# Kernel optimization log

Measured on AMD Instinct MI355X. Metric: run time of the kernel, lower is better.

The kernel has to match this reference:

```python
import jax, jax.numpy as jnp
import numpy as np

B, N, IN, H = 8, 2048, 256, 128
ALPHA = 0.2  # leaky relu slope


def setup_inputs() -> dict:
    key = jax.random.key(0)
    k1, k2, k3, k4 = jax.random.split(key, 4)
    x = jax.random.normal(k1, (B, N, IN), dtype=jnp.float32)
    # adj_identity: batched identity matrix (masks self-attention, then re-adds weight-1 self loop)
    adj_identity = jnp.broadcast_to(jnp.eye(N, dtype=jnp.float32), (B, N, N))
    W = jax.random.normal(k2, (H, IN), dtype=jnp.float32) * (1.0 / np.sqrt(IN))
    b = jnp.zeros((H,), dtype=jnp.float32)
    # atten_fact: [2H, 1], xavier_normal with gain=1.414
    std = 1.414 * np.sqrt(2.0 / (2 * H + 1))
    a = jax.random.normal(k3, (2 * H, 1), dtype=jnp.float32) * std
    return {"input": x, "adj_identity": adj_identity, "W": W, "b": b, "a": a}


def reference(input, adj_identity, W, b, a):
    # input projection: [B,N,H]
    h = jnp.einsum("bni,hi->bnh", input, W) + b
    # decomposition of cat([h_i, h_j]) @ a == h_i@a1 + h_j@a2 (exact same math,
    # avoids materializing the [B, N*N, 2H] tensor)
    a1 = a[:H, 0]  # [H]
    a2 = a[H:, 0]  # [H]
    si = h @ a1  # [B,N]
    sj = h @ a2  # [B,N]
    scores = jax.nn.leaky_relu(si[:, :, None] + sj[:, None, :], negative_slope=ALPHA)  # [B,N,N]
    scores = jnp.where(adj_identity != 0, -jnp.inf, scores)
    attn = jax.nn.softmax(scores, axis=-1) + adj_identity  # [B,N,N]
    # dropout p=0.0 -> identity
    out = jax.nn.elu(jnp.einsum("bnm,bmh->bnh", attn, h))
    return out
```

## Files before the change

### kernel.cpp

```cpp
#include <hip/hip_runtime.h>
#include <hip/hip_bf16.h>
#include <cmath>


#define ALPHA 0.2f
#define NN 2048
#define NIN 256
#define NH 128

typedef __attribute__((ext_vector_type(8))) short short8;
typedef __attribute__((ext_vector_type(4))) float f32x4;

__device__ __forceinline__ unsigned int pk2(float a, float b) {
    unsigned int r;
    asm("v_cvt_pk_bf16_f32 %0, %1, %2" : "=v"(r) : "v"(a), "v"(b));
    return r;
}

__global__ __launch_bounds__(256) void k1_h(
    const float* __restrict__ x, const float* __restrict__ Wm,
    const float* __restrict__ bias, const float* __restrict__ av,
    float* __restrict__ si, float* __restrict__ sj,
    unsigned short* __restrict__ hTt)
{
    __shared__ __align__(16) unsigned short xls[64 * 264];
    __shared__ __align__(16) unsigned short Wls[128 * 264];
    __shared__ float a1l[128], a2l[128], bl[128];

    const int t = threadIdx.x;
    const int r0 = blockIdx.x * 64;

    for (int p = 0; p < 16; ++p) {
        int idx = p * 256 + t;
        int row = idx >> 6, kq = idx & 63;
        f32x4 v = *(const f32x4*)(x + (size_t)(r0 + row) * NIN + kq * 4);
        *(uint2*)(&xls[row * 264 + kq * 4]) = make_uint2(pk2(v[0], v[1]), pk2(v[2], v[3]));
    }
    for (int p = 0; p < 32; ++p) {
        int idx = p * 256 + t;
        int row = idx >> 6, kq = idx & 63;
        f32x4 v = *(const f32x4*)(Wm + (size_t)row * NIN + kq * 4);
        *(uint2*)(&Wls[row * 264 + kq * 4]) = make_uint2(pk2(v[0], v[1]), pk2(v[2], v[3]));
    }
    if (t < 128) { a1l[t] = av[t]; a2l[t] = av[128 + t]; bl[t] = bias[t]; }
    __syncthreads();

    const int w = t >> 6, l = t & 63, la = l & 15, g = l >> 4;

    f32x4 acc[8];
#pragma unroll
    for (int n = 0; n < 8; ++n) acc[n] = (f32x4){0.f, 0.f, 0.f, 0.f};

#pragma unroll
    for (int ks = 0; ks < 8; ++ks) {
        short8 af = *(const short8*)(&xls[(w * 16 + la) * 264 + ks * 32 + g * 8]);
#pragma unroll
        for (int n = 0; n < 8; ++n) {
            short8 bfr = *(const short8*)(&Wls[(n * 16 + la) * 264 + ks * 32 + g * 8]);
            acc[n] = __builtin_amdgcn_mfma_f32_16x16x32_bf16(af, bfr, acc[n], 0, 0, 0);
        }
    }

    float s1[4] = {0.f, 0.f, 0.f, 0.f}, s2[4] = {0.f, 0.f, 0.f, 0.f};
#pragma unroll
    for (int n = 0; n < 8; ++n) {
        int col = n * 16 + la;
#pragma unroll
        for (int r = 0; r < 4; ++r) {
            float v = acc[n][r] + bl[col];
            acc[n][r] = v;
            s1[r] += v * a1l[col];
            s2[r] += v * a2l[col];
        }
    }
#pragma unroll
    for (int r = 0; r < 4; ++r) {
#pragma unroll
        for (int m = 1; m < 16; m <<= 1) {
            s1[r] += __shfl_xor(s1[r], m, 64);
            s2[r] += __shfl_xor(s2[r], m, 64);
        }
    }
    if (la == 0) {
#pragma unroll
        for (int r = 0; r < 4; ++r) {
            int row = w * 16 + g * 4 + r;
            si[r0 + row] = s1[r];
            sj[r0 + row] = s2[r];
        }
    }

    __syncthreads();
    unsigned short* oT = xls;
#pragma unroll
    for (int n = 0; n < 8; ++n) {
        int col = n * 16 + la;
        int row0 = w * 16 + g * 4;
        *(uint2*)(&oT[col * 72 + row0]) =
            make_uint2(pk2(acc[n][0], acc[n][1]), pk2(acc[n][2], acc[n][3]));
    }
    __syncthreads();
    const int b = r0 >> 11, jt = (r0 & (NN - 1)) >> 6;
    unsigned short* dst = hTt + ((size_t)(b * 32 + jt)) * 8192;
    for (int p = 0; p < 4; ++p) {
        int idx = p * 256 + t;
        int col = idx >> 3, seg = idx & 7;
        uint4 v = *(const uint4*)(&oT[col * 72 + seg * 8]);
        *(uint4*)(dst + col * 64 + seg * 8) = v;
    }
}

__global__ __launch_bounds__(512) void k3_attn(
    const unsigned short* __restrict__ hTt,
    const float* __restrict__ si, const float* __restrict__ sj,
    float* __restrict__ out)
{
    __shared__ __align__(16) float f1l[NN];
    __shared__ __align__(16) float f2l[NN];
    __shared__ __align__(16) unsigned short hl[2][128 * 72];
    __shared__ float Zl[2][32];
    __shared__ float mr1[8], mr2[8];

    const int t = threadIdx.x;
    const int bb = blockIdx.x & 7;
    const int grp = blockIdx.x >> 3;
    const int i0 = grp * 32;
    const int w = t >> 6, l = t & 63;
    const int wr = (w >> 2) & 1;
    const int wcg = (w >> 1) & 1;
    const int wk = w & 1;
    const int la = l & 15, g = l >> 4;

    const unsigned short* tb = hTt + (size_t)bb * (32 * 8192);

    uint4 c0 = ((const uint4*)tb)[t];
    uint4 c1 = ((const uint4*)tb)[t + 512];

    ((f32x4*)f1l)[t] = ((const f32x4*)(sj + bb * NN))[t];
    __syncthreads();
    f32x4 vv = ((const f32x4*)f1l)[t];
    float m1, m2;
    {
        float hi0 = fmaxf(vv[0], vv[1]), lo0 = fminf(vv[0], vv[1]);
        float hi1 = fmaxf(vv[2], vv[3]), lo1 = fminf(vv[2], vv[3]);
        m1 = fmaxf(hi0, hi1);
        m2 = fmaxf(fminf(hi0, hi1), fmaxf(lo0, lo1));
    }
#pragma unroll
    for (int m = 1; m < 64; m <<= 1) {
        float o1 = __shfl_xor(m1, m, 64), o2 = __shfl_xor(m2, m, 64);
        float n1 = fmaxf(m1, o1);
        float n2 = fmaxf(fminf(m1, o1), fmaxf(m2, o2));
        m1 = n1; m2 = n2;
    }
    if (l == 0) { mr1[w] = m1; mr2[w] = m2; }
    __syncthreads();
    {
        float a1 = mr1[0], a2 = mr2[0];
#pragma unroll
        for (int wv2 = 1; wv2 < 8; ++wv2) {
            float b1 = mr1[wv2], b2 = mr2[wv2];
            float n1 = fmaxf(a1, b1), n2 = fmaxf(fminf(a1, b1), fmaxf(a2, b2));
            a1 = n1; a2 = n2;
        }
        m1 = a1; m2 = a2;
    }
    {
        f32x4 e1t, e2t;
#pragma unroll
        for (int u = 0; u < 4; ++u) { e1t[u] = expf(vv[u]); e2t[u] = expf(ALPHA * vv[u]); }
        ((f32x4*)f1l)[t] = e1t;
        ((f32x4*)f2l)[t] = e2t;
    }

    float e1v, e2v, owv;
    {
        int gi = bb * NN + i0 + wr * 16 + la;
        float svi = si[gi], svj = sj[gi];
        float M = (svj == m1) ? m2 : m1;
        float sm = svi + M;
        float mm = sm > 0.f ? sm : ALPHA * sm;
        float a = expf(svi - mm), b2 = expf(ALPHA * svi - mm);
        e1v = a; e2v = b2;
        float owr = fmaxf(a * expf(svj), b2 * expf(ALPHA * svj));
        owv = __uint_as_float(pk2(owr, owr) << 16);
    }

    f32x4 acc[4], zac;
    zac = (f32x4){0.f, 0.f, 0.f, 0.f};
#pragma unroll
    for (int n = 0; n < 4; ++n) acc[n] = (f32x4){0.f, 0.f, 0.f, 0.f};
    short8 ones;
#pragma unroll
    for (int u = 0; u < 8; ++u) ones[u] = (short)0x3F80;

    const int sidx0 = (t >> 3) * 72 + (t & 7) * 8;
    const int sidx1 = ((t + 512) >> 3) * 72 + (t & 7) * 8;

    for (int jt = 0; jt < 32; ++jt) {
        unsigned short* buf = hl[jt & 1];
        *(uint4*)(&buf[sidx0]) = c0;
        *(uint4*)(&buf[sidx1]) = c1;
        if (jt < 31) {
            const uint4* nt = (const uint4*)(tb + (size_t)(jt + 1) * 8192);
            c0 = nt[t];
            c1 = nt[t + 512];
        }
        __syncthreads();

        const int jb = jt * 64 + wk * 32 + g * 8;
        f32x4 F1a = *(const f32x4*)(f1l + jb);
        f32x4 F1b = *(const f32x4*)(f1l + jb + 4);
        f32x4 F2a = *(const f32x4*)(f2l + jb);
        f32x4 F2b = *(const f32x4*)(f2l + jb + 4);

        short8 af;
        {
            float w0 = fmaxf(e1v * F1a[0], e2v * F2a[0]);
            float w1 = fmaxf(e1v * F1a[1], e2v * F2a[1]);
            float w2 = fmaxf(e1v * F1a[2], e2v * F2a[2]);
            float w3 = fmaxf(e1v * F1a[3], e2v * F2a[3]);
            float w4 = fmaxf(e1v * F1b[0], e2v * F2b[0]);
            float w5 = fmaxf(e1v * F1b[1], e2v * F2b[1]);
            float w6 = fmaxf(e1v * F1b[2], e2v * F2b[2]);
            float w7 = fmaxf(e1v * F1b[3], e2v * F2b[3]);
            union { unsigned int u[4]; short8 s; } cv;
            cv.u[0] = pk2(w0, w1);
            cv.u[1] = pk2(w2, w3);
            cv.u[2] = pk2(w4, w5);
            cv.u[3] = pk2(w6, w7);
            af = cv.s;
        }
#pragma unroll
        for (int n = 0; n < 4; ++n) {
            const int col = wcg * 64 + n * 16 + la;
            short8 bfr = *(const short8*)(&buf[col * 72 + wk * 32 + g * 8]);
            acc[n] = __builtin_amdgcn_mfma_f32_16x16x32_bf16(af, bfr, acc[n], 0, 0, 0);
        }
        zac = __builtin_amdgcn_mfma_f32_16x16x32_bf16(af, ones, zac, 0, 0, 0);
    }

    __syncthreads();
    float* xch = (float*)hl;
    const int pair = wr * 2 + wcg;
    if (wk == 1) {
#pragma unroll
        for (int n = 0; n < 4; ++n)
#pragma unroll
            for (int r = 0; r < 4; ++r)
                xch[(n * 4 + r) * 256 + pair * 64 + l] = acc[n][r];
    }
    if (wcg == 0 && la == 0) {
#pragma unroll
        for (int r = 0; r < 4; ++r)
            Zl[wk][wr * 16 + g * 4 + r] = zac[r];
    }
    __syncthreads();

    if (wk == 0) {
#pragma unroll
        for (int n = 0; n < 4; ++n)
#pragma unroll
            for (int r = 0; r < 4; ++r)
                acc[n][r] += xch[(n * 4 + r) * 256 + pair * 64 + l];

        const int jt_res = grp >> 1;
        const int joff = (grp & 1) * 32;
#pragma unroll
        for (int n = 0; n < 4; ++n) {
            const int col = wcg * 64 + n * 16 + la;
#pragma unroll
            for (int r = 0; r < 4; ++r) {
                const int row = wr * 16 + g * 4 + r;
                const float Z = Zl[0][row] + Zl[1][row];
                const int srcl = (g * 4 + r) | (l & 48);
                const float owq = __shfl(owv, srcl, 64);
                const float hv = __uint_as_float(
                    (unsigned int)tb[jt_res * 8192 + col * 64 + joff + row] << 16);
                const float num = acc[n][r] - owq * hv;
                const float den = Z - owq;
                float o = num / den + hv;
                out[(size_t)(bb * NN + i0 + row) * NH + col] = o > 0.f ? o : expm1f(o);
            }
        }
    }
}

extern "C" void kernel_launch(void* const* d_in, const int* in_sizes, int n_in,
                              void* d_out, int out_size, void* d_ws, size_t ws_size,
                              hipStream_t stream)
{
    const float* x    = (const float*)d_in[0];
    const float* Wm   = (const float*)d_in[2];
    const float* bias = (const float*)d_in[3];
    const float* av   = (const float*)d_in[4];
    float* out = (float*)d_out;

    float* wsf = (float*)d_ws;
    unsigned short* hTt = (unsigned short*)wsf;
    float* si = wsf + 1048576;
    float* sj = wsf + 1064960;

    hipLaunchKernelGGL(k1_h,    dim3(256), dim3(256), 0, stream, x, Wm, bias, av, si, sj, hTt);
    hipLaunchKernelGGL(k3_attn, dim3(512), dim3(512), 0, stream, hTt, si, sj, out);
}
```

Measured before the change: 40.60 us.

## Split projection kernel across 8 waves by output column and stage W in halves

The projection kernel now runs 512 threads per block, with each wave owning 16 output columns across all 64 rows instead of 16 rows across all columns. W is converted and staged into shared memory in two K-halves to cut LDS footprint. The si/sj dot products are reduced across waves through a new shared buffer. This adds parallelism and lowers LDS use in the small first kernel, at the cost of an extra barrier and a cross-wave reduction.

```diff
diff --git a/kernel.cpp b/kernel.cpp
--- a/kernel.cpp
+++ b/kernel.cpp
@@ -17,96 +17,108 @@
     return r;
 }
 
-__global__ __launch_bounds__(256) void k1_h(
+__global__ __launch_bounds__(512) void k1_h(
     const float* __restrict__ x, const float* __restrict__ Wm,
     const float* __restrict__ bias, const float* __restrict__ av,
     float* __restrict__ si, float* __restrict__ sj,
     unsigned short* __restrict__ hTt)
 {
     __shared__ __align__(16) unsigned short xls[64 * 264];
-    __shared__ __align__(16) unsigned short Wls[128 * 264];
+    __shared__ __align__(16) unsigned short Wh[128 * 136];
     __shared__ float a1l[128], a2l[128], bl[128];
+    __shared__ float red1[8][64], red2[8][64];
 
     const int t = threadIdx.x;
     const int r0 = blockIdx.x * 64;
-
-    for (int p = 0; p < 16; ++p) {
-        int idx = p * 256 + t;
+    const int w = t >> 6, l = t & 63, la = l & 15, g = l >> 4;
+
+    for (int i = 0; i < 8; ++i) {
+        int idx = i * 512 + t;
         int row = idx >> 6, kq = idx & 63;
         f32x4 v = *(const f32x4*)(x + (size_t)(r0 + row) * NIN + kq * 4);
         *(uint2*)(&xls[row * 264 + kq * 4]) = make_uint2(pk2(v[0], v[1]), pk2(v[2], v[3]));
     }
-    for (int p = 0; p < 32; ++p) {
-        int idx = p * 256 + t;
-        int row = idx >> 6, kq = idx & 63;
-        f32x4 v = *(const f32x4*)(Wm + (size_t)row * NIN + kq * 4);
-        *(uint2*)(&Wls[row * 264 + kq * 4]) = make_uint2(pk2(v[0], v[1]), pk2(v[2], v[3]));
-    }
     if (t < 128) { a1l[t] = av[t]; a2l[t] = av[128 + t]; bl[t] = bias[t]; }
-    __syncthreads();
-
-    const int w = t >> 6, l = t & 63, la = l & 15, g = l >> 4;
-
-    f32x4 acc[8];
-#pragma unroll
-    for (int n = 0; n < 8; ++n) acc[n] = (f32x4){0.f, 0.f, 0.f, 0.f};
-
-#pragma unroll
-    for (int ks = 0; ks < 8; ++ks) {
-        short8 af = *(const short8*)(&xls[(w * 16 + la) * 264 + ks * 32 + g * 8]);
-#pragma unroll
-        for (int n = 0; n < 8; ++n) {
-            short8 bfr = *(const short8*)(&Wls[(n * 16 + la) * 264 + ks * 32 + g * 8]);
-            acc[n] = __builtin_amdgcn_mfma_f32_16x16x32_bf16(af, bfr, acc[n], 0, 0, 0);
-        }
-    }
-
-    float s1[4] = {0.f, 0.f, 0.f, 0.f}, s2[4] = {0.f, 0.f, 0.f, 0.f};
-#pragma unroll
-    for (int n = 0; n < 8; ++n) {
-        int col = n * 16 + la;
+
+    f32x4 acc[4];
+#pragma unroll
+    for (int fr = 0; fr < 4; ++fr) acc[fr] = (f32x4){0.f, 0.f, 0.f, 0.f};
+
+#pragma unroll
+    for (int kh = 0; kh < 2; ++kh) {
+        if (kh) __syncthreads();
+        for (int i = 0; i < 8; ++i) {
+            int idx = i * 512 + t;
+            int row = idx >> 5, kq = idx & 31;
+            f32x4 v = *(const f32x4*)(Wm + (size_t)row * NIN + kh * 128 + kq * 4);
+            *(uint2*)(&Wh[row * 136 + kq * 4]) = make_uint2(pk2(v[0], v[1]), pk2(v[2], v[3]));
+        }
+        __syncthreads();
+#pragma unroll
+        for (int ksl = 0; ksl < 4; ++ksl) {
+            short8 bfr = *(const short8*)(&Wh[(w * 16 + la) * 136 + ksl * 32 + g * 8]);
+#pragma unroll
+            for (int fr = 0; fr < 4; ++fr) {
+                short8 af = *(const short8*)(
+                    &xls[(fr * 16 + la) * 264 + kh * 128 + ksl * 32 + g * 8]);
+                acc[fr] = __builtin_amdgcn_mfma_f32_16x16x32_bf16(af, bfr, acc[fr], 0, 0, 0);
+            }
+        }
+    }
+
+    const int col = w * 16 + la;
+    float s1[4][4], s2[4][4];
+#pragma unroll
+    for (int fr = 0; fr < 4; ++fr)
 #pragma unroll
         for (int r = 0; r < 4; ++r) {
-            float v = acc[n][r] + bl[col];
-            acc[n][r] = v;
-            s1[r] += v * a1l[col];
-            s2[r] += v * a2l[col];
-        }
-    }
-#pragma unroll
-    for (int r = 0; r < 4; ++r) {
-#pragma unroll
-        for (int m = 1; m < 16; m <<= 1) {
-            s1[r] += __shfl_xor(s1[r], m, 64);
-            s2[r] += __shfl_xor(s2[r], m, 64);
-        }
-    }
+            float v = acc[fr][r] + bl[col];
+            acc[fr][r] = v;
+            s1[fr][r] = v * a1l[col];
+            s2[fr][r] = v * a2l[col];
+        }
+#pragma unroll
+    for (int m = 1; m < 16; m <<= 1)
+#pragma unroll
+        for (int fr = 0; fr < 4; ++fr)
+#pragma unroll
+            for (int r = 0; r < 4; ++r) {
+                s1[fr][r] += __shfl_xor(s1[fr][r], m, 64);
+                s2[fr][r] += __shfl_xor(s2[fr][r], m, 64);
+            }
     if (la == 0) {
 #pragma unroll
-        for (int r = 0; r < 4; ++r) {
-            int row = w * 16 + g * 4 + r;
-            si[r0 + row] = s1[r];
-            sj[r0 + row] = s2[r];
-        }
-    }
-
-    __syncthreads();
+        for (int fr = 0; fr < 4; ++fr)
+#pragma unroll
+            for (int r = 0; r < 4; ++r) {
+                red1[w][fr * 16 + g * 4 + r] = s1[fr][r];
+                red2[w][fr * 16 + g * 4 + r] = s2[fr][r];
+            }
+    }
+    __syncthreads();
+
     unsigned short* oT = xls;
 #pragma unroll
-    for (int n = 0; n < 8; ++n) {
-        int col = n * 16 + la;
-        int row0 = w * 16 + g * 4;
-        *(uint2*)(&oT[col * 72 + row0]) =
-            make_uint2(pk2(acc[n][0], acc[n][1]), pk2(acc[n][2], acc[n][3]));
-    }
-    __syncthreads();
+    for (int fr = 0; fr < 4; ++fr) {
+        *(uint2*)(&oT[col * 72 + fr * 16 + g * 4]) =
+            make_uint2(pk2(acc[fr][0], acc[fr][1]), pk2(acc[fr][2], acc[fr][3]));
+    }
+    __syncthreads();
+
     const int b = r0 >> 11, jt = (r0 & (NN - 1)) >> 6;
-    unsigned short* dst = hTt + ((size_t)(b * 32 + jt)) * 8192;
-    for (int p = 0; p < 4; ++p) {
-        int idx = p * 256 + t;
-        int col = idx >> 3, seg = idx & 7;
-        uint4 v = *(const uint4*)(&oT[col * 72 + seg * 8]);
-        *(uint4*)(dst + col * 64 + seg * 8) = v;
+    unsigned short* dst = hTt + (size_t)(b * 32 + jt) * 8192;
+    for (int i = 0; i < 2; ++i) {
+        int idx = i * 512 + t;
+        int c2 = idx >> 3, seg = idx & 7;
+        uint4 v = *(const uint4*)(&oT[c2 * 72 + seg * 8]);
+        *(uint4*)(dst + c2 * 64 + seg * 8) = v;
+    }
+    if (t < 64) {
+        float a = 0.f, b2 = 0.f;
+#pragma unroll
+        for (int w2 = 0; w2 < 8; ++w2) { a += red1[w2][t]; b2 += red2[w2][t]; }
+        si[r0 + t] = a;
+        sj[r0 + t] = b2;
     }
 }
 
@@ -301,6 +313,6 @@
     float* si = wsf + 1048576;
     float* sj = wsf + 1064960;
 
-    hipLaunchKernelGGL(k1_h,    dim3(256), dim3(256), 0, stream, x, Wm, bias, av, si, sj, hTt);
+    hipLaunchKernelGGL(k1_h,    dim3(256), dim3(512), 0, stream, x, Wm, bias, av, si, sj, hTt);
     hipLaunchKernelGGL(k3_attn, dim3(512), dim3(512), 0, stream, hTt, si, sj, out);
 }
```

Result: slower. 42.84 us (+5.5%).
